# Kernel tuning notes

Hardware: AMD Instinct MI355X
Metric: run time of the kernel (lower is better)

Reference implementation:

```python
import jax, jax.numpy as jnp
import numpy as np
from jax import lax

MIN_LEVEL, MAX_LEVEL = 2, 6
IMG_H, IMG_W = 832, 1344
B = 2
A = 3              # anchors per location: 3 aspect ratios x 1 scale
C = 256            # FPN channels
PRE_NMS = 1000     # rpn test pre_nms_topn (per level)
POST_NMS = 1000    # rpn test post_nms_topn (final rois)
NMS_THRESH = 0.7
NUM_CLASSES = 91
MLP_DIM = 1024
BBOX_CLIP = float(np.log(1000.0 / 16.0))
LEVELS = list(range(MIN_LEVEL, MAX_LEVEL + 1))
HW = {l: (IMG_H // 2**l, IMG_W // 2**l) for l in LEVELS}


def _make_anchors(level):
    H, W = HW[level]
    stride = 2.0**level
    base = 8.0 * stride                      # anchor.scale = 8
    ars = np.array([1.0, 2.0, 0.5])
    ah, aw = base / np.sqrt(ars), base * np.sqrt(ars)   # [A]
    cy = (np.arange(H) + 0.5) * stride
    cx = (np.arange(W) + 0.5) * stride
    y1 = cy[:, None, None] - ah / 2.0        # [H,1,A]
    y2 = cy[:, None, None] + ah / 2.0
    x1 = cx[None, :, None] - aw / 2.0        # [1,W,A]
    x2 = cx[None, :, None] + aw / 2.0
    anc = np.stack(np.broadcast_arrays(y1, x1, y2, x2), -1)  # [H,W,A,4]
    return anc.reshape(-1, 4).astype(np.float32)


def _decode(anc, d):
    ah = anc[..., 2] - anc[..., 0]
    aw = anc[..., 3] - anc[..., 1]
    acy = anc[..., 0] + 0.5 * ah
    acx = anc[..., 1] + 0.5 * aw
    dy, dx = d[..., 0], d[..., 1]
    dh = jnp.minimum(d[..., 2], BBOX_CLIP)
    dw = jnp.minimum(d[..., 3], BBOX_CLIP)
    cy = acy + dy * ah
    cx = acx + dx * aw
    h = ah * jnp.exp(dh)
    w = aw * jnp.exp(dw)
    return jnp.stack([cy - 0.5 * h, cx - 0.5 * w, cy + 0.5 * h, cx + 0.5 * w], -1)


def _iou_matrix(b):
    area = jnp.maximum(b[:, 2] - b[:, 0], 0.0) * jnp.maximum(b[:, 3] - b[:, 1], 0.0)
    yy1 = jnp.maximum(b[:, None, 0], b[None, :, 0])
    xx1 = jnp.maximum(b[:, None, 1], b[None, :, 1])
    yy2 = jnp.minimum(b[:, None, 2], b[None, :, 2])
    xx2 = jnp.minimum(b[:, None, 3], b[None, :, 3])
    inter = jnp.maximum(yy2 - yy1, 0.0) * jnp.maximum(xx2 - xx1, 0.0)
    return inter / (area[:, None] + area[None, :] - inter + 1e-8)


def _nms_keep(boxes):
    # greedy NMS on score-sorted boxes, fixed iteration count (jit-safe)
    n = boxes.shape[0]
    iou = _iou_matrix(boxes)
    idx = jnp.arange(n)
    def body(i, keep):
        sup = (iou[i] > NMS_THRESH) & (idx > i) & keep[i]
        return keep & (~sup)
    return lax.fori_loop(0, n, body, jnp.ones((n,), bool))


def _propose_level(score, delta, anc, img_hw):
    b = score.shape[0]
    s = jax.nn.sigmoid(score.reshape(b, -1))
    boxes = _decode(anc[None], delta.reshape(b, -1, 4))
    hmax = img_hw[:, 0][:, None]
    wmax = img_hw[:, 1][:, None]
    boxes = jnp.stack([jnp.clip(boxes[..., 0], 0.0, hmax),
                       jnp.clip(boxes[..., 1], 0.0, wmax),
                       jnp.clip(boxes[..., 2], 0.0, hmax),
                       jnp.clip(boxes[..., 3], 0.0, wmax)], -1)
    n = min(PRE_NMS, s.shape[1])
    ts, ti = lax.top_k(s, n)                               # sorted desc
    tb = jnp.take_along_axis(boxes, ti[..., None], axis=1)
    keep = jax.vmap(_nms_keep)(lax.stop_gradient(tb))
    return jnp.where(keep, ts, -1.0), tb


def _roi_align(feats, boxes, out_size=7):
    # multilevel crop-and-resize: sample 2*out_size grid bilinearly from the
    # FPN level assigned by the standard heuristic, then 2x2 avg pool.
    b = feats[0].shape[0]
    Hs = jnp.array([f.shape[1] for f in feats], jnp.int32)
    Ws = jnp.array([f.shape[2] for f in feats], jnp.int32)
    offs = jnp.array(np.concatenate([[0], np.cumsum([f.shape[1] * f.shape[2] for f in feats])[:-1]]), jnp.int32)
    strides = jnp.array([2.0**l for l in LEVELS], jnp.float32)
    flat = jnp.concatenate([f.reshape(b, -1, C) for f in feats], axis=1)  # [B,T,C]
    S = 2 * out_size
    t = jnp.arange(S, dtype=jnp.float32) / (S - 1)

    def one(fb, box):
        y1, x1, y2, x2 = box[0], box[1], box[2], box[3]
        area = jnp.maximum(y2 - y1, 0.0) * jnp.maximum(x2 - x1, 0.0)
        lvl = jnp.clip(jnp.floor(4.0 + jnp.log2(jnp.sqrt(area) / 224.0 + 1e-8)), MIN_LEVEL, MAX_LEVEL).astype(jnp.int32)
        li = lvl - MIN_LEVEL
        Hl, Wl, off, sc = Hs[li], Ws[li], offs[li], strides[li]
        ys = jnp.clip((y1 + (y2 - y1) * t) / sc, 0.0, Hl.astype(jnp.float32) - 1.0)
        xs = jnp.clip((x1 + (x2 - x1) * t) / sc, 0.0, Wl.astype(jnp.float32) - 1.0)
        y0 = jnp.floor(ys).astype(jnp.int32); y1i = jnp.minimum(y0 + 1, Hl - 1)
        x0 = jnp.floor(xs).astype(jnp.int32); x1i = jnp.minimum(x0 + 1, Wl - 1)
        wy = (ys - y0)[:, None, None]
        wx = (xs - x0)[None, :, None]
        g = lambda yy, xx: fb[off + yy[:, None] * Wl + xx[None, :]]   # [S,S,C]
        v = (g(y0, x0) * (1 - wy) * (1 - wx) + g(y0, x1i) * (1 - wy) * wx
             + g(y1i, x0) * wy * (1 - wx) + g(y1i, x1i) * wy * wx)
        return v.reshape(out_size, 2, out_size, 2, C).mean(axis=(1, 3))

    return jax.vmap(lambda fb, bxs: jax.vmap(lambda bx: one(fb, bx))(bxs))(flat, boxes)


def _forward(feats, scores, deltas, ancs, image_info, w1, b1, w2, b2, wc, bc, wb, bb):
    img_hw = image_info[:, :2]
    ss, bs = [], []
    for sc_, dl_, an_ in zip(scores, deltas, ancs):
        s_, b_ = _propose_level(sc_, dl_, an_, img_hw)
        ss.append(s_); bs.append(b_)
    all_s = jnp.concatenate(ss, axis=1)
    all_b = jnp.concatenate(bs, axis=1)
    rs, ri = lax.top_k(all_s, POST_NMS)
    rois = jnp.take_along_axis(all_b, ri[..., None], axis=1)   # [B,R,4]
    rois = lax.stop_gradient(rois)                              # as in training path
    roi_feats = _roi_align(feats, rois, 7)                      # [B,R,7,7,C]
    x = roi_feats.reshape(roi_feats.shape[0], roi_feats.shape[1], -1)
    h1 = jax.nn.relu(x @ w1 + b1)
    h2 = jax.nn.relu(h1 @ w2 + b2)
    return h2 @ wc + bc, h2 @ wb + bb, rois, rs


def setup_inputs() -> dict:
    key = jax.random.key(0)
    ks = jax.random.split(key, 24)
    inp = {}
    for i, l in enumerate(LEVELS):
        H, W = HW[l]
        inp[f"feat{l}"] = jax.random.normal(ks[i], (B, H, W, C), jnp.float32)
        inp[f"score{l}"] = jax.random.normal(ks[5 + i], (B, H, W, A), jnp.float32)
        inp[f"delta{l}"] = jax.random.normal(ks[10 + i], (B, H, W, 4 * A), jnp.float32) * 0.1
        inp[f"anc{l}"] = jnp.asarray(_make_anchors(l))
    inp["image_info"] = jnp.tile(jnp.array([[IMG_H, IMG_W, 1.0, IMG_H, IMG_W]], jnp.float32), (B, 1))
    D = 7 * 7 * C
    inp["w1"] = jax.random.normal(ks[15], (D, MLP_DIM), jnp.float32) * 0.01
    inp["b1"] = jnp.zeros((MLP_DIM,), jnp.float32)
    inp["w2"] = jax.random.normal(ks[16], (MLP_DIM, MLP_DIM), jnp.float32) * 0.02
    inp["b2"] = jnp.zeros((MLP_DIM,), jnp.float32)
    inp["wc"] = jax.random.normal(ks[17], (MLP_DIM, NUM_CLASSES), jnp.float32) * 0.02
    inp["bc"] = jnp.zeros((NUM_CLASSES,), jnp.float32)
    inp["wb"] = jax.random.normal(ks[18], (MLP_DIM, 4 * NUM_CLASSES), jnp.float32) * 0.02
    inp["bb"] = jnp.zeros((4 * NUM_CLASSES,), jnp.float32)
    return inp


def reference(feat2, feat3, feat4, feat5, feat6,
              score2, score3, score4, score5, score6,
              delta2, delta3, delta4, delta5, delta6,
              anc2, anc3, anc4, anc5, anc6,
              image_info, w1, b1, w2, b2, wc, bc, wb, bb):
    return _forward([feat2, feat3, feat4, feat5, feat6],
                    [score2, score3, score4, score5, score6],
                    [delta2, delta3, delta4, delta5, delta6],
                    [anc2, anc3, anc4, anc5, anc6],
                    image_info, w1, b1, w2, b2, wc, bc, wb, bb)
```

## Files before the change

### kernel.cpp

```cpp
#include <hip/hip_runtime.h>
#include <hip/hip_bf16.h>
#include <math.h>

typedef unsigned int u32;
typedef unsigned long long u64;
typedef unsigned short u16;
typedef __bf16 bf16x8 __attribute__((ext_vector_type(8)));
typedef float f32x4 __attribute__((ext_vector_type(4)));

#define DEV __device__ __forceinline__

DEV u32 okey(float f){ u32 u=__float_as_uint(f); return (u & 0x80000000u) ? ~u : (u | 0x80000000u); }
DEV float unokey(u32 v){ u32 u = (v & 0x80000000u) ? (v & 0x7FFFFFFFu) : ~v; return __uint_as_float(u); }
DEV u16 f2bf(float f){ u32 u=__float_as_uint(f); u32 r = u + 0x7FFFu + ((u>>16)&1u); return (u16)(r>>16); }

DEV void stage16(const void* g, void* l){
  __builtin_amdgcn_global_load_lds((const __attribute__((address_space(1))) void*)g,
                                   (__attribute__((address_space(3))) void*)l, 16, 0, 0);
}

__constant__ const int c_Nls[5] = {209664,52416,13104,3276,819};
__constant__ const int c_nss[5] = {1000,1000,1000,1000,819};

__global__ __launch_bounds__(256) void k_castT(const float* __restrict__ src, u16* __restrict__ dst, int K, int N){
  __shared__ float tile[32][33];
  int bk = blockIdx.x, bn = blockIdx.y;
  int tx = threadIdx.x, ty = threadIdx.y;
  #pragma unroll
  for (int i=0;i<4;i++){
    int r = bk*32 + ty + i*8;
    tile[ty+i*8][tx] = src[(size_t)r*N + bn*32 + tx];
  }
  __syncthreads();
  #pragma unroll
  for (int i=0;i<4;i++){
    int n = bn*32 + ty + i*8;
    dst[(size_t)n*K + bk*32 + tx] = f2bf(tile[tx][ty+i*8]);
  }
}

__global__ __launch_bounds__(256) void k_castW3(const float* __restrict__ wc, const float* __restrict__ wb,
    const float* __restrict__ bc, const float* __restrict__ bb,
    u16* __restrict__ BT3, float* __restrict__ bias3){
  int idx = blockIdx.x*256 + threadIdx.x;
  int n = idx >> 10, k = idx & 1023;
  float v = 0.f;
  if (n < 91) v = wc[(size_t)k*91 + n];
  else if (n < 455) v = wb[(size_t)k*364 + (n-91)];
  BT3[(size_t)n*1024 + k] = f2bf(v);
  if (idx < 512){
    float bv = 0.f;
    if (idx < 91) bv = bc[idx]; else if (idx < 455) bv = bb[idx-91];
    bias3[idx] = bv;
  }
}

__global__ __launch_bounds__(256) void k_zero(u32* __restrict__ p, int n){
  int i = blockIdx.x*256 + threadIdx.x;
  if (i < n) p[i] = 0u;
}

__global__ __launch_bounds__(256) void k_hist(const float* s2,const float* s3,const float* s4,const float* s5,const float* s6,
    u32* __restrict__ histG){
  int grp = blockIdx.x >> 6, blk = blockIdx.x & 63;
  int li = grp % 5, b = grp / 5;
  const float* sp = (li==0?s2: li==1?s3: li==2?s4: li==3?s5: s6) + (size_t)b*c_Nls[li];
  int Nl = c_Nls[li];
  __shared__ u32 h[2048];
  int tid = threadIdx.x;
  for (int i=tid;i<2048;i+=256) h[i]=0u;
  __syncthreads();
  for (int i = blk*256 + tid; i < Nl; i += 64*256){
    u32 u = okey(sp[i]);
    atomicAdd(&h[u >> 21], 1u);
  }
  __syncthreads();
  u32* hg = histG + grp*2048;
  for (int i=tid;i<2048;i+=256){ u32 v=h[i]; if (v) atomicAdd(&hg[i], v); }
}

__global__ __launch_bounds__(256) void k_select(const u32* __restrict__ histG, u32* __restrict__ thrG){
  int grp = blockIdx.x;
  int li = grp % 5;
  u32 ns = (u32)c_nss[li];
  const u32* hg = histG + grp*2048;
  __shared__ u32 part[256];
  int tid = threadIdx.x;
  int hibase = 2047 - tid*8;
  u32 s = 0;
  #pragma unroll
  for (int j=0;j<8;j++) s += hg[hibase - j];
  part[tid] = s;
  __syncthreads();
  if (tid==0){
    u32 cum = 0; int t;
    for (t=0;t<255;t++){ if (cum + part[t] >= ns) break; cum += part[t]; }
    int hb = 2047 - t*8;
    int bin = hb - 7;
    for (int j=0;j<8;j++){ u32 c = hg[hb-j]; if (cum + c >= ns){ bin = hb-j; break; } cum += c; }
    thrG[grp] = (u32)bin;
  }
}

__global__ __launch_bounds__(256) void k_gather(const float* s2,const float* s3,const float* s4,const float* s5,const float* s6,
    const u32* __restrict__ thrG, u32* __restrict__ cntG, u64* __restrict__ cand){
  int grp = blockIdx.x >> 6, blk = blockIdx.x & 63;
  int li = grp % 5, b = grp / 5;
  const float* sp = (li==0?s2: li==1?s3: li==2?s4: li==3?s5: s6) + (size_t)b*c_Nls[li];
  int Nl = c_Nls[li];
  u32 T = thrG[grp] << 21;
  for (int i = blk*256 + threadIdx.x; i < Nl; i += 64*256){
    u32 u = okey(sp[i]);
    if (u >= T){
      u32 pos = atomicAdd(&cntG[grp], 1u);
      if (pos < 2048u) cand[(size_t)grp*2048 + pos] = ((u64)u<<32) | (u32)(~(u32)i);
    }
  }
}

__global__ __launch_bounds__(256) void k_sortC(const u64* __restrict__ cand, const u32* __restrict__ cntG,
    u32* __restrict__ selIdx, float* __restrict__ sRaw, float* __restrict__ sPre){
  int grp = blockIdx.x;
  int li = grp % 5, b = grp / 5;
  int ns = c_nss[li];
  __shared__ u64 keys[2048];
  int tid = threadIdx.x;
  u32 cnt = cntG[grp]; if (cnt > 2048u) cnt = 2048u;
  for (int i=tid;i<2048;i+=256) keys[i] = (i < (int)cnt) ? cand[(size_t)grp*2048 + i] : 0ull;
  for (int k2=2;k2<=2048;k2<<=1){
    for (int j2=k2>>1;j2>=1;j2>>=1){
      __syncthreads();
      for (int t=tid;t<1024;t+=256){
        int i1 = ((t & ~(j2-1))<<1) | (t & (j2-1));
        int i2 = i1 | j2;
        u64 a=keys[i1], bb2=keys[i2];
        bool asc = (i1 & k2) != 0;
        bool sw = asc ? (a>bb2) : (a<bb2);
        if (sw){ keys[i1]=bb2; keys[i2]=a; }
      }
    }
  }
  __syncthreads();
  int base = b*4819 + li*1000;
  for (int r=tid;r<ns;r+=256){
    u64 kk = keys[r];
    u32 idx = ~((u32)kk);
    float scv = unokey((u32)(kk>>32));
    selIdx[base+r] = idx;
    sRaw[base+r] = scv;
    sPre[base+r] = (float)(1.0/(1.0+exp(-(double)scv)));
  }
}

__global__ __launch_bounds__(256) void k_decode(const u32* __restrict__ selIdx,
    const float* a2,const float* a3,const float* a4,const float* a5,const float* a6,
    const float* d2,const float* d3,const float* d4,const float* d5,const float* d6,
    const float* __restrict__ info, float* __restrict__ boxes){
  int g = blockIdx.x*256 + threadIdx.x;
  if (g >= 9638) return;
  int b = g/4819, r = g%4819;
  int li = r/1000; if (li>4) li=4;
  u32 idx = selIdx[g];
  const float* anc = li==0?a2: li==1?a3: li==2?a4: li==3?a5: a6;
  const float* del = li==0?d2: li==1?d3: li==2?d4: li==3?d5: d6;
  const float* aa = anc + (size_t)idx*4;
  const float* dd = del + ((size_t)b*c_Nls[li] + idx)*4;
  float ah=aa[2]-aa[0], aw=aa[3]-aa[1];
  float acy=aa[0]+0.5f*ah, acx=aa[1]+0.5f*aw;
  const float CLIPV = 4.135166556742356f;
  float dh=fminf(dd[2],CLIPV), dw=fminf(dd[3],CLIPV);
  float cy=acy+dd[0]*ah, cx=acx+dd[1]*aw;
  float hh=ah*expf(dh), ww=aw*expf(dw);
  float hmax=info[b*5+0], wmax=info[b*5+1];
  float vy1=fminf(fmaxf(cy-0.5f*hh,0.f),hmax);
  float vx1=fminf(fmaxf(cx-0.5f*ww,0.f),wmax);
  float vy2=fminf(fmaxf(cy+0.5f*hh,0.f),hmax);
  float vx2=fminf(fmaxf(cx+0.5f*ww,0.f),wmax);
  ((float4*)boxes)[g] = make_float4(vy1,vx1,vy2,vx2);
}

__global__ __launch_bounds__(256) void k_nms_mask(const float* __restrict__ boxes, u64* __restrict__ masks){
  int rg = blockIdx.x;
  int b = rg/4819, r = rg%4819;
  int li = r/1000; if (li>4) li=4;
  int i = r - li*1000;
  int n = c_nss[li];
  int gb = b*4819 + li*1000;
  __shared__ float4 sbi;
  if (threadIdx.x==0) sbi = ((const float4*)boxes)[gb+i];
  __syncthreads();
  float4 bi = sbi;
  float ai = fmaxf(bi.z-bi.x,0.f)*fmaxf(bi.w-bi.y,0.f);
  int t = threadIdx.x, wv = t>>6, lane = t&63;
  #pragma unroll
  for (int it=0; it<4; ++it){
    int jj = it*256 + wv*64 + lane;
    bool c = false;
    if (jj < n && jj > i){
      float4 bj = ((const float4*)boxes)[gb+jj];
      float aj = fmaxf(bj.z-bj.x,0.f)*fmaxf(bj.w-bj.y,0.f);
      float yy1=fmaxf(bi.x,bj.x), xx1=fmaxf(bi.y,bj.y);
      float yy2=fminf(bi.z,bj.z), xx2=fminf(bi.w,bj.w);
      float inter=fmaxf(yy2-yy1,0.f)*fmaxf(xx2-xx1,0.f);
      float iou = inter/(ai+aj-inter+1e-8f);
      c = iou > 0.7f;
    }
    u64 m = __ballot(c);
    if (lane==0) masks[(size_t)rg*16 + it*4 + wv] = m;
  }
}

__global__ __launch_bounds__(64) void k_nms_reduce(const u64* __restrict__ masks, const float* __restrict__ sPre, float* __restrict__ allS){
  int li = blockIdx.x % 5, b = blockIdx.x / 5;
  int n = c_nss[li];
  int gb = b*4819 + li*1000;
  int lane = threadIdx.x;
  bool ld = lane < 16;
  const u64* mrow = masks + (size_t)gb*16;
  u64 removed = 0ull, rpiv = 0ull;

  u64 ownA[8], pivA[8], ownB[8], pivB[8], ownC[8], pivC[8], ownD[8], pivD[8];

#define LOADC(c0, own, piv) do{ \
  _Pragma("unroll") \
  for (int r_=0;r_<8;r_++){ \
    int i_=(c0)*8+r_; \
    bool ok_ = i_<n; \
    own[r_] = (ok_&&ld) ? mrow[(size_t)i_*16 + lane] : 0ull; \
    piv[r_] = ok_ ? mrow[(size_t)i_*16 + (i_>>6)] : 0ull; \
  } }while(0)

#define RESYNC(c0) do{ \
  if (((c0)&7)==0 && (c0)>0 && (c0)*8 < n) rpiv = __shfl(removed, (c0)>>3); \
  }while(0)

#define PROC(c0, own, piv) do{ \
  RESYNC(c0); \
  _Pragma("unroll") \
  for (int r_=0;r_<8;r_++){ \
    int i_=(c0)*8+r_; \
    if (i_<n){ \
      bool kept_ = ((rpiv >> (i_&63)) & 1ull) == 0ull; \
      if (kept_){ removed |= own[r_]; rpiv |= piv[r_]; } \
    } \
  } }while(0)

  int nc = (n+7)>>3;
  LOADC(0, ownA, pivA);
  LOADC(1, ownB, pivB);
  LOADC(2, ownC, pivC);
  LOADC(3, ownD, pivD);
  for (int c=0; c<nc; c+=4){
    PROC(c,   ownA, pivA); LOADC(c+4, ownA, pivA);
    PROC(c+1, ownB, pivB); LOADC(c+5, ownB, pivB);
    PROC(c+2, ownC, pivC); LOADC(c+6, ownC, pivC);
    PROC(c+3, ownD, pivD); LOADC(c+7, ownD, pivD);
  }
#undef LOADC
#undef RESYNC
#undef PROC

  if (lane < 16){
    for (int q=0; q<64; ++q){
      int jj = lane*64 + q;
      if (jj < n){
        bool kp = ((removed >> q) & 1ull) == 0ull;
        allS[gb+jj] = kp ? sPre[gb+jj] : -1.0f;
      }
    }
  }
}

__global__ __launch_bounds__(1024) void k_final(const float* __restrict__ allS, const float* __restrict__ sRaw,
   const float* __restrict__ boxes, float* __restrict__ outR, float* __restrict__ outS){
  __shared__ u64 keys[8192];
  int b = blockIdx.x, tid = threadIdx.x;
  for (int e=tid;e<8192;e+=1024){
    u64 kk = 0ull;
    if (e < 4819){
      float v = allS[b*4819+e];
      u32 ie = (~(u32)e) & 0x7FFFFFFFu;
      if (v > -0.5f) kk = (1ull<<63) | ((u64)okey(sRaw[b*4819+e])<<31) | (u64)ie;
      else           kk = (u64)ie;
    }
    keys[e] = kk;
  }
  for (int k2=2;k2<=8192;k2<<=1){
    for (int j2=k2>>1;j2>=1;j2>>=1){
      __syncthreads();
      for (int t=tid;t<4096;t+=1024){
        int i1 = ((t & ~(j2-1))<<1) | (t & (j2-1));
        int i2 = i1 | j2;
        u64 a=keys[i1], bb2=keys[i2];
        bool asc = (i1 & k2) != 0;
        bool sw = asc ? (a>bb2) : (a<bb2);
        if (sw){ keys[i1]=bb2; keys[i2]=a; }
      }
    }
  }
  __syncthreads();
  for (int r=tid;r<1000;r+=1024){
    u64 kk = keys[r];
    u32 ieF = (u32)kk & 0x7FFFFFFFu;
    int e = (int)((~ieF) & 0x7FFFFFFFu);
    outS[b*1000+r] = allS[b*4819+e];
    ((float4*)outR)[b*1000+r] = ((const float4*)boxes)[b*4819+e];
  }
}

__global__ __launch_bounds__(256) void k_roi(const float* __restrict__ rois,
    const float* f2,const float* f3,const float* f4,const float* f5,const float* f6,
    u16* __restrict__ Amat){
  constexpr int Hs[5]={208,104,52,26,13};
  constexpr int Wsv[5]={336,168,84,42,21};
  constexpr float strd[5]={4.f,8.f,16.f,32.f,64.f};
  int g = blockIdx.x;
  u16* Arow = Amat + (size_t)g*12544;
  int tid = threadIdx.x;
  if (g >= 2000){
    for (int i=tid;i<12544;i+=256) Arow[i]=0;
    return;
  }
  int b = g/1000;
  const float* box = rois + (size_t)g*4;
  float y1=box[0], x1=box[1], y2=box[2], x2=box[3];
  float area = fmaxf(y2-y1,0.f)*fmaxf(x2-x1,0.f);
  int lvl = (int)floorf(4.f + log2f(sqrtf(area)/224.f + 1e-8f));
  lvl = lvl < 2 ? 2 : (lvl > 6 ? 6 : lvl);
  int li = lvl-2;
  int Hl=Hs[li], Wl=Wsv[li]; float sc=strd[li];
  __shared__ float swy[14], swx[14];
  __shared__ int sy0[14], sy1[14], sx0[14], sx1[14];
  if (tid < 14){
    float t = (float)tid / 13.f;
    float ys = (y1 + (y2-y1)*t)/sc; ys = fminf(fmaxf(ys,0.f),(float)(Hl-1));
    int yy0 = (int)floorf(ys);
    sy0[tid]=yy0; sy1[tid]=(yy0+1>Hl-1)?(Hl-1):(yy0+1); swy[tid]=ys-(float)yy0;
    float xs = (x1 + (x2-x1)*t)/sc; xs = fminf(fmaxf(xs,0.f),(float)(Wl-1));
    int xx0 = (int)floorf(xs);
    sx0[tid]=xx0; sx1[tid]=(xx0+1>Wl-1)?(Wl-1):(xx0+1); swx[tid]=xs-(float)xx0;
  }
  __syncthreads();
  const float* fb = (li==0?f2: li==1?f3: li==2?f4: li==3?f5: f6) + (size_t)b*Hl*Wl*256;
  int c = tid;
  for (int cell=0; cell<49; ++cell){
    int cy=cell/7, cx=cell%7;
    float accv=0.f;
    #pragma unroll
    for (int sy=0;sy<2;sy++){
      int iy=cy*2+sy;
      float wy=swy[iy];
      const float* r0 = fb + (size_t)sy0[iy]*Wl*256;
      const float* r1 = fb + (size_t)sy1[iy]*Wl*256;
      #pragma unroll
      for (int sx=0;sx<2;sx++){
        int ix=cx*2+sx;
        float wx=swx[ix];
        int xa=sx0[ix]*256+c, xb=sx1[ix]*256+c;
        float v00=r0[xa], v01=r0[xb], v10=r1[xa], v11=r1[xb];
        accv += v00*(1.f-wy)*(1.f-wx) + v01*(1.f-wy)*wx + v10*wy*(1.f-wx) + v11*wy*wx;
      }
    }
    Arow[cell*256+c] = f2bf(accv*0.25f);
  }
}

template<int EPI>
__global__ __launch_bounds__(256) void k_gemm(const u16* __restrict__ A, const u16* __restrict__ BT,
    const float* __restrict__ bias, u16* __restrict__ Hh,
    float* __restrict__ out0, float* __restrict__ out1,
    int K, int nTileN, int nk){
  __shared__ __align__(16) char lds[24576];
  char* ldsA = lds;
  char* ldsB = lds + 16384;
  int bid = blockIdx.x;
  int nwg = gridDim.x;
  int q = nwg >> 3;
  int wgid = (bid & 7)*q + (bid >> 3);
  int mi = wgid / nTileN, ni = wgid % nTileN;
  int m0 = mi*128, n0 = ni*64;
  int tid = threadIdx.x;
  int w = tid >> 6, lane = tid & 63;
  int wm = w >> 1, wn = w & 1;
  int lo4 = lane & 15, hi2 = lane >> 4, xr = lane & 7;
  f32x4 acc[4][2];
  #pragma unroll
  for (int m=0;m<4;m++)
    #pragma unroll
    for (int n=0;n<2;n++) acc[m][n] = (f32x4){0.f,0.f,0.f,0.f};
  int wavebase = tid & ~63;
  for (int kt=0; kt<nk; ++kt){
    const u16* Ak = A + (size_t)kt*64;
    const u16* Bk = BT + (size_t)kt*64;
    #pragma unroll
    for (int c=0;c<4;c++){
      int flat = c*256 + tid;
      int prow = flat >> 3;
      int ls = (flat & 7) ^ (prow & 7);
      stage16(Ak + (size_t)(m0+prow)*K + ls*8, ldsA + (size_t)(c*256 + wavebase)*16);
    }
    #pragma unroll
    for (int c=0;c<2;c++){
      int flat = c*256 + tid;
      int prow = flat >> 3;
      int ls = (flat & 7) ^ (prow & 7);
      stage16(Bk + (size_t)(n0+prow)*K + ls*8, ldsB + (size_t)(c*256 + wavebase)*16);
    }
    __syncthreads();
    bf16x8 af[2][4], bfv[2][2];
    #pragma unroll
    for (int ks=0;ks<2;ks++){
      int sA = (((ks*4 + hi2) ^ xr) << 4);
      #pragma unroll
      for (int m=0;m<4;m++) af[ks][m] = *(const bf16x8*)(ldsA + (wm*64 + m*16 + lo4)*128 + sA);
      #pragma unroll
      for (int n=0;n<2;n++) bfv[ks][n] = *(const bf16x8*)(ldsB + (wn*32 + n*16 + lo4)*128 + sA);
    }
    #pragma unroll
    for (int ks=0;ks<2;ks++)
      #pragma unroll
      for (int m=0;m<4;m++)
        #pragma unroll
        for (int n=0;n<2;n++)
          acc[m][n] = __builtin_amdgcn_mfma_f32_16x16x32_bf16(af[ks][m], bfv[ks][n], acc[m][n], 0,0,0);
    __syncthreads();
  }
  #pragma unroll
  for (int m=0;m<4;m++){
    #pragma unroll
    for (int n=0;n<2;n++){
      int col = n0 + wn*32 + n*16 + lo4;
      float bv = bias[col];
      int rbase = m0 + wm*64 + m*16 + hi2*4;
      #pragma unroll
      for (int j=0;j<4;j++){
        float v = acc[m][n][j] + bv;
        int rr = rbase + j;
        if (EPI == 0){
          v = fmaxf(v, 0.f);
          Hh[(size_t)rr*1024 + col] = f2bf(v);
        } else {
          if (rr < 2000){
            if (col < 91) out0[(size_t)rr*91 + col] = v;
            else if (col < 455) out1[(size_t)rr*364 + (col-91)] = v;
          }
        }
      }
    }
  }
}

extern "C" void kernel_launch(void* const* d_in, const int* in_sizes, int n_in,
                              void* d_out, int out_size, void* d_ws, size_t ws_size,
                              hipStream_t stream) {
  (void)in_sizes; (void)n_in; (void)out_size; (void)ws_size;
  const float *f[5], *s[5], *dl[5], *an[5];
  for (int i=0;i<5;i++){
    f[i]  = (const float*)d_in[4*i+0];
    s[i]  = (const float*)d_in[4*i+1];
    dl[i] = (const float*)d_in[4*i+2];
    an[i] = (const float*)d_in[4*i+3];
  }
  const float* info = (const float*)d_in[20];
  const float* w1 = (const float*)d_in[21];
  const float* b1 = (const float*)d_in[22];
  const float* w2 = (const float*)d_in[23];
  const float* b2 = (const float*)d_in[24];
  const float* wc = (const float*)d_in[25];
  const float* bc = (const float*)d_in[26];
  const float* wb = (const float*)d_in[27];
  const float* bbp= (const float*)d_in[28];

  char* base = (char*)d_ws; size_t off = 0;
  auto alloc = [&](size_t bytes)->char*{ char* p = base + off; off = (off + bytes + 255) & ~(size_t)255; return p; };
  u16*  BT1   = (u16*)alloc(1024ull*12544*2);
  u16*  BT2   = (u16*)alloc(1024ull*1024*2);
  u16*  BT3   = (u16*)alloc(512ull*1024*2);
  float* bias3= (float*)alloc(512*4);
  u16*  Amat  = (u16*)alloc(2048ull*12544*2);
  u16*  h1    = (u16*)alloc(2048ull*1024*2);
  u16*  h2    = (u16*)alloc(2048ull*1024*2);
  u32*  selIdx= (u32*)alloc(9638ull*4);
  float* sRaw = (float*)alloc(9638ull*4);
  float* sPre = (float*)alloc(9638ull*4);
  float* boxes= (float*)alloc(9638ull*16);
  float* allS = (float*)alloc(9638ull*4);
  u64*  masks = (u64*)alloc(9638ull*16*8);
  u32*  histG = (u32*)alloc(10ull*2048*4);
  u32*  cntG  = (u32*)alloc(64);
  u32*  thrG  = (u32*)alloc(64);
  u64*  cand  = (u64*)alloc(10ull*2048*8);

  float* out0 = (float*)d_out;
  float* out1 = out0 + 182000;
  float* outR = out0 + 910000;
  float* outS = out0 + 918000;

  k_castT<<<dim3(392,32), dim3(32,8), 0, stream>>>(w1, BT1, 12544, 1024);
  k_castT<<<dim3(32,32),  dim3(32,8), 0, stream>>>(w2, BT2, 1024, 1024);
  k_castW3<<<dim3(2048), dim3(256), 0, stream>>>(wc, wb, bc, bbp, BT3, bias3);

  k_zero<<<dim3(82), dim3(256), 0, stream>>>(histG, 10*2048 + 32);
  k_hist<<<dim3(640), dim3(256), 0, stream>>>(s[0],s[1],s[2],s[3],s[4], histG);
  k_select<<<dim3(10), dim3(256), 0, stream>>>(histG, thrG);
  k_gather<<<dim3(640), dim3(256), 0, stream>>>(s[0],s[1],s[2],s[3],s[4], thrG, cntG, cand);
  k_sortC<<<dim3(10), dim3(256), 0, stream>>>(cand, cntG, selIdx, sRaw, sPre);

  k_decode<<<dim3(38), dim3(256), 0, stream>>>(selIdx,
      an[0],an[1],an[2],an[3],an[4], dl[0],dl[1],dl[2],dl[3],dl[4], info, boxes);
  k_nms_mask<<<dim3(9638), dim3(256), 0, stream>>>(boxes, masks);
  k_nms_reduce<<<dim3(10), dim3(64), 0, stream>>>(masks, sPre, allS);
  k_final<<<dim3(2), dim3(1024), 0, stream>>>(allS, sRaw, boxes, outR, outS);
  k_roi<<<dim3(2048), dim3(256), 0, stream>>>(outR, f[0],f[1],f[2],f[3],f[4], Amat);
  k_gemm<0><<<dim3(256), dim3(256), 0, stream>>>(Amat, BT1, b1, h1, nullptr, nullptr, 12544, 16, 196);
  k_gemm<0><<<dim3(256), dim3(256), 0, stream>>>(h1,   BT2, b2, h2, nullptr, nullptr, 1024, 16, 16);
  k_gemm<1><<<dim3(128), dim3(256), 0, stream>>>(h2,   BT3, bias3, nullptr, out0, out1, 1024, 8, 16);
}
```

Before: 921.5 us.

## Split-K the first MLP GEMM four ways with a separate reduce+ReLU kernel

```diff
diff --git a/kernel.cpp b/kernel.cpp
--- a/kernel.cpp
+++ b/kernel.cpp
@@ -450,6 +450,97 @@
   }
 }
 
+__global__ __launch_bounds__(256) void k_gemm_sk(const u16* __restrict__ A, const u16* __restrict__ BT,
+    float* __restrict__ Cpart, int K, int nTileN, int nTiles, int nkPer){
+  __shared__ __align__(16) char lds[24576];
+  char* ldsA = lds;
+  char* ldsB = lds + 16384;
+  int bid = blockIdx.x;
+  int nwg = gridDim.x;
+  int q = nwg >> 3;
+  int wgid = (bid & 7)*q + (bid >> 3);
+  int kidx = wgid / nTiles;
+  int rem  = wgid - kidx*nTiles;
+  int mi = rem / nTileN, ni = rem % nTileN;
+  int m0 = mi*128, n0 = ni*64;
+  int kbase = kidx * nkPer * 64;
+  int tid = threadIdx.x;
+  int w = tid >> 6, lane = tid & 63;
+  int wm = w >> 1, wn = w & 1;
+  int lo4 = lane & 15, hi2 = lane >> 4, xr = lane & 7;
+  f32x4 acc[4][2];
+  #pragma unroll
+  for (int m=0;m<4;m++)
+    #pragma unroll
+    for (int n=0;n<2;n++) acc[m][n] = (f32x4){0.f,0.f,0.f,0.f};
+  int wavebase = tid & ~63;
+  for (int kt=0; kt<nkPer; ++kt){
+    const u16* Ak = A + (size_t)(kbase + kt*64);
+    const u16* Bk = BT + (size_t)(kbase + kt*64);
+    #pragma unroll
+    for (int c=0;c<4;c++){
+      int flat = c*256 + tid;
+      int prow = flat >> 3;
+      int ls = (flat & 7) ^ (prow & 7);
+      stage16(Ak + (size_t)(m0+prow)*K + ls*8, ldsA + (size_t)(c*256 + wavebase)*16);
+    }
+    #pragma unroll
+    for (int c=0;c<2;c++){
+      int flat = c*256 + tid;
+      int prow = flat >> 3;
+      int ls = (flat & 7) ^ (prow & 7);
+      stage16(Bk + (size_t)(n0+prow)*K + ls*8, ldsB + (size_t)(c*256 + wavebase)*16);
+    }
+    __syncthreads();
+    bf16x8 af[2][4], bfv[2][2];
+    #pragma unroll
+    for (int ks=0;ks<2;ks++){
+      int sA = (((ks*4 + hi2) ^ xr) << 4);
+      #pragma unroll
+      for (int m=0;m<4;m++) af[ks][m] = *(const bf16x8*)(ldsA + (wm*64 + m*16 + lo4)*128 + sA);
+      #pragma unroll
+      for (int n=0;n<2;n++) bfv[ks][n] = *(const bf16x8*)(ldsB + (wn*32 + n*16 + lo4)*128 + sA);
+    }
+    #pragma unroll
+    for (int ks=0;ks<2;ks++)
+      #pragma unroll
+      for (int m=0;m<4;m++)
+        #pragma unroll
+        for (int n=0;n<2;n++)
+          acc[m][n] = __builtin_amdgcn_mfma_f32_16x16x32_bf16(af[ks][m], bfv[ks][n], acc[m][n], 0,0,0);
+    __syncthreads();
+  }
+  float* Cp = Cpart + ((size_t)kidx << 21);
+  #pragma unroll
+  for (int m=0;m<4;m++){
+    #pragma unroll
+    for (int n=0;n<2;n++){
+      int col = n0 + wn*32 + n*16 + lo4;
+      int rbase = m0 + wm*64 + m*16 + hi2*4;
+      #pragma unroll
+      for (int j=0;j<4;j++){
+        Cp[(size_t)(rbase+j)*1024 + col] = acc[m][n][j];
+      }
+    }
+  }
+}
+
+__global__ __launch_bounds__(256) void k_redrelu(const float* __restrict__ Cpart,
+    const float* __restrict__ bias, u16* __restrict__ Hh){
+  int idx = (blockIdx.x*256 + threadIdx.x)*4;
+  float4 p0 = *(const float4*)(Cpart + idx);
+  float4 p1 = *(const float4*)(Cpart + (1u<<21) + idx);
+  float4 p2 = *(const float4*)(Cpart + (2u<<21) + idx);
+  float4 p3 = *(const float4*)(Cpart + (3u<<21) + idx);
+  float4 bv = *(const float4*)(bias + (idx & 1023));
+  ushort4 o;
+  o.x = f2bf(fmaxf(p0.x+p1.x+p2.x+p3.x+bv.x, 0.f));
+  o.y = f2bf(fmaxf(p0.y+p1.y+p2.y+p3.y+bv.y, 0.f));
+  o.z = f2bf(fmaxf(p0.z+p1.z+p2.z+p3.z+bv.z, 0.f));
+  o.w = f2bf(fmaxf(p0.w+p1.w+p2.w+p3.w+bv.w, 0.f));
+  *(ushort4*)(Hh + idx) = o;
+}
+
 extern "C" void kernel_launch(void* const* d_in, const int* in_sizes, int n_in,
                               void* d_out, int out_size, void* d_ws, size_t ws_size,
                               hipStream_t stream) {
@@ -490,6 +581,7 @@
   u32*  cntG  = (u32*)alloc(64);
   u32*  thrG  = (u32*)alloc(64);
   u64*  cand  = (u64*)alloc(10ull*2048*8);
+  float* Cpart= (float*)alloc(4ull*2048*1024*4);
 
   float* out0 = (float*)d_out;
   float* out1 = out0 + 182000;
@@ -512,7 +604,10 @@
   k_nms_reduce<<<dim3(10), dim3(64), 0, stream>>>(masks, sPre, allS);
   k_final<<<dim3(2), dim3(1024), 0, stream>>>(allS, sRaw, boxes, outR, outS);
   k_roi<<<dim3(2048), dim3(256), 0, stream>>>(outR, f[0],f[1],f[2],f[3],f[4], Amat);
-  k_gemm<0><<<dim3(256), dim3(256), 0, stream>>>(Amat, BT1, b1, h1, nullptr, nullptr, 12544, 16, 196);
+
+  k_gemm_sk<<<dim3(1024), dim3(256), 0, stream>>>(Amat, BT1, Cpart, 12544, 16, 256, 49);
+  k_redrelu<<<dim3(2048), dim3(256), 0, stream>>>(Cpart, b1, h1);
+
   k_gemm<0><<<dim3(256), dim3(256), 0, stream>>>(h1,   BT2, b2, h2, nullptr, nullptr, 1024, 16, 16);
   k_gemm<1><<<dim3(128), dim3(256), 0, stream>>>(h2,   BT3, bias3, nullptr, out0, out1, 1024, 8, 16);
 }
```

Result: faster. 806.1 us (-12.5%).
